# Performance work log

Hardware: AMD Instinct MI355X
Metric: run time of the kernel (lower is better)

Reference implementation:

```python
import jax, jax.numpy as jnp
import numpy as np

B, C, N, K = 8, 128, 16384, 8


def setup_inputs() -> dict:
    key = jax.random.key(0)
    ks = jax.random.split(key, 20)
    s = 1.0 / np.sqrt(C)
    def mat(k_, shape, scale):
        return jax.random.normal(k_, shape, jnp.float32) * scale
    return {
        "x": jax.random.normal(ks[0], (B, C, N, 1), jnp.float32),
        "logits": jax.random.normal(ks[1], (B, N), jnp.float32),
        "Wq1": mat(ks[2], (C, C), s), "Wk1": mat(ks[3], (C, C), s), "Wv1": mat(ks[4], (C, C), s),
        "Wq2": mat(ks[5], (C, C), s), "Wk2": mat(ks[6], (C, C), s), "Wv2": mat(ks[7], (C, C), s),
        "Wq3": mat(ks[8], (C, C), s), "Wk3": mat(ks[9], (C, C), s), "Wv3": mat(ks[10], (C, C), s),
        "ln_w": jnp.ones((C,), jnp.float32), "ln_b": jnp.zeros((C,), jnp.float32),
        "conv0_w": mat(ks[11], (C, C), s), "conv0_b": jnp.zeros((C,), jnp.float32),
        "bn_w": jnp.ones((C,), jnp.float32), "bn_b": jnp.zeros((C,), jnp.float32),
        "fc1_w": mat(ks[12], (C // 2, C), s), "fc1_b": jnp.zeros((C // 2,), jnp.float32),
        "fc2_w": mat(ks[13], (C, C // 2), 1.0 / np.sqrt(C // 2)), "fc2_b": jnp.zeros((C,), jnp.float32),
        "k": K,
    }


def _transformer(f, Wq, Wk, Wv):
    # f: [B, C, n] ; 1x1 convs over channel dim
    q = jnp.einsum('oc,bcn->bon', Wq, f)
    kk = jnp.einsum('oc,bcn->bon', Wk, f)
    v = jnp.einsum('oc,bcn->bon', Wv, f)
    temp = jnp.sqrt(jnp.asarray(f.shape[1], f.dtype))
    attn = jax.nn.softmax(jnp.einsum('bcn,bdn->bcd', q / temp, kk), axis=-1)  # [B,C,C]
    return jnp.einsum('bcd,bdn->bcn', attn, v)


def _layernorm_over_c(f, w, b):
    # f: [B, C, n]; original transposes to [B, n, C], LayerNorm(C, eps=1e-6), back
    ft = jnp.swapaxes(f, 1, 2)
    mu = ft.mean(-1, keepdims=True)
    var = ft.var(-1, keepdims=True)
    ft = (ft - mu) * jax.lax.rsqrt(var + 1e-6) * w + b
    return jnp.swapaxes(ft, 1, 2)


def reference(x, logits, Wq1, Wk1, Wv1, Wq2, Wk2, Wv2, Wq3, Wk3, Wv3,
              ln_w, ln_b, conv0_w, conv0_b, bn_w, bn_b, fc1_w, fc1_b, fc2_w, fc2_b, k):
    # --- tanh-threshold binning into k buckets ---
    w = jnp.tanh(logits)                       # [B, N]
    flag = 2.0 / k
    lows = -1.0 + flag * jnp.arange(k, dtype=x.dtype)   # [k]
    highs = lows + flag
    wb = w[None, :, :]                         # [1, B, N]
    # transforto0_1: in (l, r], and original zeros stay zero
    masks = ((wb > lows[:, None, None]) & (wb <= highs[:, None, None]) & (wb != 0)).astype(x.dtype)  # [k,B,N]
    nums = masks.sum(-1)                       # [k, B]
    nums = jnp.where(nums == 0, 1.0, nums)

    x2 = x[..., 0]                             # [B, C, N]
    # masked segment pooling (mean per bin), no channel-broadcast repeat
    pooled = jnp.einsum('bcn,kbn->bck', x2, masks)        # [B, C, k]
    feature = pooled / nums.T[:, None, :]                 # [B, C, k]

    # --- three tiny attention blocks with residual + LN ---
    for Wq, Wk, Wv in ((Wq1, Wk1, Wv1), (Wq2, Wk2, Wv2), (Wq3, Wk3, Wv3)):
        out = _transformer(feature, Wq, Wk, Wv) + feature
        feature = _layernorm_over_c(out, ln_w, ln_b)

    # --- scatter-add reconstruction: sum_i mask_i*x + mask_i*level_i ---
    total = masks.sum(0)                                  # [B, N]
    recon = x2 * total[:, None, :] + jnp.einsum('bck,kbn->bcn', feature, masks)
    result = recon[..., None]                             # [B, C, N, 1]

    # --- SE block ---
    mu_i = result.mean(axis=(2, 3), keepdims=True)
    var_i = result.var(axis=(2, 3), keepdims=True)
    h = (result - mu_i) * jax.lax.rsqrt(var_i + 1e-5)     # InstanceNorm2d
    mu_b = h.mean(axis=(0, 2, 3), keepdims=True)
    var_b = h.var(axis=(0, 2, 3), keepdims=True)
    h = (h - mu_b) * jax.lax.rsqrt(var_b + 1e-5)          # BatchNorm2d (batch stats)
    h = h * bn_w[None, :, None, None] + bn_b[None, :, None, None]
    h = jax.nn.gelu(h, approximate=False)
    conv = jnp.einsum('oc,bcnp->bonp', conv0_w, h) + conv0_b[None, :, None, None]
    sq = conv.reshape(conv.shape[0], conv.shape[1], -1).mean(-1)   # [B, C]
    f1 = jax.nn.gelu(sq @ fc1_w.T + fc1_b, approximate=False)
    f2 = jax.nn.sigmoid(f1 @ fc2_w.T + fc2_b)
    return conv * f2[:, :, None, None]
```

## Files before the change

### kernel.cpp

```cpp
#include <hip/hip_runtime.h>
#include <math.h>

#define Bdim 8
#define Cdim 128
#define Ndim 16384
#define Kdim 8

typedef __attribute__((ext_vector_type(8))) short short8;
typedef __attribute__((ext_vector_type(4))) float f32x4;

__global__ void __launch_bounds__(256) k_bin(const float* __restrict__ logits,
                                             signed char* __restrict__ kbin,
                                             int* __restrict__ cnt) {
  __shared__ int h[Kdim];
  int tid = threadIdx.x;
  if (tid < Kdim) h[tid] = 0;
  __syncthreads();
  int idx = blockIdx.x * 256 + tid;
  int b = idx >> 14;
  float w = tanhf(logits[idx]);
  int kb = -1;
#pragma unroll
  for (int j = 0; j < Kdim; ++j) {
    float lo = -1.0f + 0.25f * (float)j;
    float hi = lo + 0.25f;
    if (w > lo && w <= hi && w != 0.0f) kb = j;
  }
  kbin[idx] = (signed char)kb;
  if (kb >= 0) atomicAdd(&h[kb], 1);
  __syncthreads();
  if (tid < Kdim) atomicAdd(&cnt[b * Kdim + tid], h[tid]);
}

__global__ void __launch_bounds__(256) k_pool(const float* __restrict__ x,
                                              const signed char* __restrict__ kbin,
                                              float* __restrict__ pooled,
                                              float* __restrict__ sxx) {
  int bc = blockIdx.x;
  int b = bc >> 7;
  const float4* xr = (const float4*)(x + (size_t)bc * Ndim);
  const char4* kr = (const char4*)(kbin + b * Ndim);
  float acc[Kdim];
#pragma unroll
  for (int j = 0; j < Kdim; ++j) acc[j] = 0.f;
  float s2 = 0.f;
  int tid = threadIdx.x;
  for (int n4 = tid; n4 < Ndim / 4; n4 += 256) {
    float4 v = xr[n4];
    char4 kb = kr[n4];
    float ve[4] = {v.x, v.y, v.z, v.w};
    signed char ke[4] = {kb.x, kb.y, kb.z, kb.w};
#pragma unroll
    for (int e = 0; e < 4; ++e) {
      float xv = ve[e];
      int kv = ke[e];
      if (kv >= 0) s2 += xv * xv;
#pragma unroll
      for (int j = 0; j < Kdim; ++j) acc[j] += (kv == j) ? xv : 0.f;
    }
  }
#pragma unroll
  for (int off = 32; off > 0; off >>= 1) {
#pragma unroll
    for (int j = 0; j < Kdim; ++j) acc[j] += __shfl_down(acc[j], off);
    s2 += __shfl_down(s2, off);
  }
  __shared__ float red[4][Kdim + 1];
  int wv = tid >> 6, ln = tid & 63;
  if (ln == 0) {
#pragma unroll
    for (int j = 0; j < Kdim; ++j) red[wv][j] = acc[j];
    red[wv][Kdim] = s2;
  }
  __syncthreads();
  if (tid < Kdim) pooled[bc * Kdim + tid] = red[0][tid] + red[1][tid] + red[2][tid] + red[3][tid];
  if (tid == Kdim) sxx[bc] = red[0][Kdim] + red[1][Kdim] + red[2][Kdim] + red[3][Kdim];
}

__global__ void __launch_bounds__(256) k_warm(
    const float* __restrict__ p0, const float* __restrict__ p1, const float* __restrict__ p2,
    const float* __restrict__ p3, const float* __restrict__ p4, const float* __restrict__ p5,
    const float* __restrict__ p6, const float* __restrict__ p7, const float* __restrict__ p8,
    float* __restrict__ dummy) {
  int g = blockIdx.x >> 3;
  int t = threadIdx.x;
  int idx = g * 256 + t;
  int m = idx >> 12;
  int w = idx & 4095;
  const float* mp = m == 0 ? p0 : m == 1 ? p1 : m == 2 ? p2 : m == 3 ? p3 : m == 4 ? p4
                  : m == 5 ? p5 : m == 6 ? p6 : m == 7 ? p7 : p8;
  float4 v = ((const float4*)mp)[w];
  float s = v.x + v.y + v.z + v.w;
#pragma unroll
  for (int off = 32; off > 0; off >>= 1) s += __shfl_down(s, off);
  if ((t & 63) == 0) dummy[blockIdx.x * 4 + (t >> 6)] = s;
}

__global__ void __launch_bounds__(1024) k_xform(
    const float* __restrict__ pooled, const int* __restrict__ cnt,
    const float* __restrict__ sxx,
    const float* __restrict__ Wq1, const float* __restrict__ Wk1, const float* __restrict__ Wv1,
    const float* __restrict__ Wq2, const float* __restrict__ Wk2, const float* __restrict__ Wv2,
    const float* __restrict__ Wq3, const float* __restrict__ Wk3, const float* __restrict__ Wv3,
    const float* __restrict__ ln_w, const float* __restrict__ ln_b,
    float* __restrict__ feat, float* __restrict__ mu_i, float* __restrict__ rs_i,
    float* __restrict__ ratio) {
  __shared__ float Wl[Cdim][132];
  __shared__ float f_l[Kdim][132], q_l[Kdim][132], kk_l[Kdim][132], v_l[Kdim][132];
  __shared__ float part[Kdim][Kdim][132];
  __shared__ float pm[Kdim][132], ps[Kdim][132];
  __shared__ float lnw_l[Cdim], lnb_l[Cdim];
  __shared__ float cnt_raw[Kdim], cnt_div[Kdim];
  __shared__ float redA[Kdim][2], redB[Kdim][2];
  int b = blockIdx.x, tid = threadIdx.x;
  int c_ = tid & 127, h_ = tid >> 7;
  int o8 = tid >> 3, j8 = tid & 7;
  const float* Wq[3] = {Wq1, Wq2, Wq3};
  const float* Wk[3] = {Wk1, Wk2, Wk3};
  const float* Wv[3] = {Wv1, Wv2, Wv3};
  float4 pf0, pf1, pf2, pf3;

#define ISSUE(P)                                            \
  do {                                                      \
    const float4* s_ = (const float4*)(P);                  \
    pf0 = s_[tid]; pf1 = s_[tid + 1024];                    \
    pf2 = s_[tid + 2048]; pf3 = s_[tid + 3072];             \
  } while (0)
#define STAGE_WRITE()                                       \
  do {                                                      \
    *(float4*)&Wl[tid >> 5][(tid & 31) * 4] = pf0;          \
    *(float4*)&Wl[(tid + 1024) >> 5][(tid & 31) * 4] = pf1; \
    *(float4*)&Wl[(tid + 2048) >> 5][(tid & 31) * 4] = pf2; \
    *(float4*)&Wl[(tid + 3072) >> 5][(tid & 31) * 4] = pf3; \
  } while (0)
#define PROJ_DOT(dst)                                              \
  do {                                                             \
    float a0 = 0.f, a1 = 0.f, a2 = 0.f, a3 = 0.f;                  \
    _Pragma("unroll 4") for (int d4 = 0; d4 < 32; d4 += 4) {       \
      float4 w0 = *(const float4*)&Wl[o8][d4 * 4];                 \
      float4 f0 = *(const float4*)&f_l[j8][d4 * 4];                \
      float4 w1 = *(const float4*)&Wl[o8][d4 * 4 + 4];             \
      float4 f1 = *(const float4*)&f_l[j8][d4 * 4 + 4];            \
      float4 w2 = *(const float4*)&Wl[o8][d4 * 4 + 8];             \
      float4 f2 = *(const float4*)&f_l[j8][d4 * 4 + 8];            \
      float4 w3 = *(const float4*)&Wl[o8][d4 * 4 + 12];            \
      float4 f3 = *(const float4*)&f_l[j8][d4 * 4 + 12];           \
      a0 = fmaf(w0.x, f0.x, a0); a0 = fmaf(w0.y, f0.y, a0);        \
      a0 = fmaf(w0.z, f0.z, a0); a0 = fmaf(w0.w, f0.w, a0);        \
      a1 = fmaf(w1.x, f1.x, a1); a1 = fmaf(w1.y, f1.y, a1);        \
      a1 = fmaf(w1.z, f1.z, a1); a1 = fmaf(w1.w, f1.w, a1);        \
      a2 = fmaf(w2.x, f2.x, a2); a2 = fmaf(w2.y, f2.y, a2);        \
      a2 = fmaf(w2.z, f2.z, a2); a2 = fmaf(w2.w, f2.w, a2);        \
      a3 = fmaf(w3.x, f3.x, a3); a3 = fmaf(w3.y, f3.y, a3);        \
      a3 = fmaf(w3.z, f3.z, a3); a3 = fmaf(w3.w, f3.w, a3);        \
    }                                                              \
    dst = (a0 + a1) + (a2 + a3);                                   \
  } while (0)

  ISSUE(Wq1);
  if (tid < Kdim) {
    int cc = cnt[b * Kdim + tid];
    cnt_raw[tid] = (float)cc;
    cnt_div[tid] = (float)(cc == 0 ? 1 : cc);
  }
  if (tid >= 128 && tid < 256) lnw_l[tid - 128] = ln_w[tid - 128];
  if (tid >= 256 && tid < 384) lnb_l[tid - 256] = ln_b[tid - 256];
  __syncthreads();
  f_l[j8][o8] = pooled[(b * Cdim + o8) * Kdim + j8] / cnt_div[j8];
  const float inv_temp = 0.08838834764831845f;
  float t_carry = 0.f;
  float sv[16];
  float mloc = 0.f;
  for (int layer = 0; layer < 3; ++layer) {
    if (layer > 0) {
      float S1 = redA[h_][0] + redA[h_][1];
      float S2 = redB[h_][0] + redB[h_][1];
      float mu = S1 * (1.f / Cdim);
      float var = S2 * (1.f / Cdim) - mu * mu;
      float rs = rsqrtf(var + 1e-6f);
      f_l[h_][c_] = (t_carry - mu) * rs * lnw_l[c_] + lnb_l[c_];
    }
    STAGE_WRITE();
    ISSUE(Wk[layer]);
    __syncthreads();
    {
      float r;
      PROJ_DOT(r);
      q_l[j8][o8] = r * inv_temp;
    }
    __syncthreads();
    STAGE_WRITE();
    ISSUE(Wv[layer]);
    __syncthreads();
    {
      float r;
      PROJ_DOT(r);
      kk_l[j8][o8] = r;
    }
    __syncthreads();
    STAGE_WRITE();
    if (layer < 2) ISSUE(Wq[layer + 1]);
    __syncthreads();
    {
      float r;
      PROJ_DOT(r);
      v_l[j8][o8] = r;
    }
    __syncthreads();
    {
      int d0 = h_ * 16;
      float qv[8];
#pragma unroll
      for (int j = 0; j < 8; ++j) qv[j] = q_l[j][c_];
#pragma unroll
      for (int dd = 0; dd < 16; ++dd) sv[dd] = 0.f;
#pragma unroll
      for (int j = 0; j < 8; ++j) {
#pragma unroll
        for (int d4 = 0; d4 < 4; ++d4) {
          float4 k4 = *(const float4*)&kk_l[j][d0 + d4 * 4];
          sv[d4 * 4 + 0] = fmaf(qv[j], k4.x, sv[d4 * 4 + 0]);
          sv[d4 * 4 + 1] = fmaf(qv[j], k4.y, sv[d4 * 4 + 1]);
          sv[d4 * 4 + 2] = fmaf(qv[j], k4.z, sv[d4 * 4 + 2]);
          sv[d4 * 4 + 3] = fmaf(qv[j], k4.w, sv[d4 * 4 + 3]);
        }
      }
      mloc = sv[0];
#pragma unroll
      for (int dd = 1; dd < 16; ++dd) mloc = fmaxf(mloc, sv[dd]);
      float sl = 0.f;
#pragma unroll
      for (int dd = 0; dd < 16; ++dd) {
        sv[dd] = expf(sv[dd] - mloc);
        sl += sv[dd];
      }
      pm[h_][c_] = mloc;
      ps[h_][c_] = sl;
    }
    __syncthreads();
    {
      float M = pm[0][c_];
#pragma unroll
      for (int hh = 1; hh < 8; ++hh) M = fmaxf(M, pm[hh][c_]);
      float S = 0.f;
#pragma unroll
      for (int hh = 0; hh < 8; ++hh) S += ps[hh][c_] * expf(pm[hh][c_] - M);
      float fac = expf(mloc - M) / S;
#pragma unroll
      for (int dd = 0; dd < 16; ++dd) sv[dd] *= fac;
      int d0 = h_ * 16;
#pragma unroll
      for (int j = 0; j < 8; ++j) {
        float po = 0.f;
#pragma unroll
        for (int d4 = 0; d4 < 4; ++d4) {
          float4 v4 = *(const float4*)&v_l[j][d0 + d4 * 4];
          po = fmaf(sv[d4 * 4 + 0], v4.x, po);
          po = fmaf(sv[d4 * 4 + 1], v4.y, po);
          po = fmaf(sv[d4 * 4 + 2], v4.z, po);
          po = fmaf(sv[d4 * 4 + 3], v4.w, po);
        }
        part[h_][j][c_] = po;
      }
    }
    __syncthreads();
    {
      float t = f_l[h_][c_];
#pragma unroll
      for (int hh = 0; hh < 8; ++hh) t += part[hh][h_][c_];
      t_carry = t;
      float s1 = t, s2 = t * t;
#pragma unroll
      for (int off = 32; off > 0; off >>= 1) {
        s1 += __shfl_xor(s1, off);
        s2 += __shfl_xor(s2, off);
      }
      int wv = (tid >> 6) & 1;
      if ((tid & 63) == 0) { redA[h_][wv] = s1; redB[h_][wv] = s2; }
    }
    __syncthreads();
  }
  {
    float S1 = redA[h_][0] + redA[h_][1];
    float S2 = redB[h_][0] + redB[h_][1];
    float mu = S1 * (1.f / Cdim);
    float var = S2 * (1.f / Cdim) - mu * mu;
    float rs = rsqrtf(var + 1e-6f);
    f_l[h_][c_] = (t_carry - mu) * rs * lnw_l[c_] + lnb_l[c_];
  }
  __syncthreads();
  if (tid < Cdim) {
    int c = tid;
    float S1 = 0.f, S2c = 0.f;
#pragma unroll
    for (int j = 0; j < Kdim; ++j) {
      float pl = pooled[(b * Cdim + c) * Kdim + j];
      float fe = f_l[j][c];
      feat[(b * Cdim + c) * Kdim + j] = fe;
      S1 += pl + cnt_raw[j] * fe;
      S2c += 2.f * pl * fe + cnt_raw[j] * fe * fe;
    }
    float S2 = sxx[b * Cdim + c] + S2c;
    float mu = S1 * (1.f / Ndim);
    float var = S2 * (1.f / Ndim) - mu * mu;
    float rs = rsqrtf(var + 1e-5f);
    mu_i[b * Cdim + c] = mu;
    rs_i[b * Cdim + c] = rs;
    ratio[b * Cdim + c] = var * rs * rs;
  }
#undef ISSUE
#undef STAGE_WRITE
#undef PROJ_DOT
}

__global__ void k_alpha(const float* __restrict__ mu_i, const float* __restrict__ rs_i,
                        const float* __restrict__ ratio, const float* __restrict__ bn_w,
                        const float* __restrict__ bn_b, float* __restrict__ alpha,
                        float* __restrict__ beta) {
  int c = threadIdx.x;
  float vb = 0.f;
  for (int b = 0; b < Bdim; ++b) vb += ratio[b * Cdim + c];
  vb *= (1.f / Bdim);
  float rsb = rsqrtf(vb + 1e-5f);
  float w = bn_w[c], bb = bn_b[c];
  for (int b = 0; b < Bdim; ++b) {
    float a = rs_i[b * Cdim + c] * rsb * w;
    alpha[b * Cdim + c] = a;
    beta[b * Cdim + c] = bb - mu_i[b * Cdim + c] * a;
  }
}

__global__ void k_wsplit(const float* __restrict__ W, unsigned short* __restrict__ Wh,
                         unsigned short* __restrict__ Wl, unsigned short* __restrict__ Whs,
                         unsigned short* __restrict__ Wls) {
  int idx = blockIdx.x * 256 + threadIdx.x;
  int o = idx >> 7, c = idx & 127;
  float v = W[idx];
  unsigned u = __float_as_uint(v);
  unsigned rh = (u + 0x7FFFu + ((u >> 16) & 1u)) & 0xFFFF0000u;
  float vh = __uint_as_float(rh);
  float r = v - vh;
  unsigned u2 = __float_as_uint(r);
  unsigned rl = (u2 + 0x7FFFu + ((u2 >> 16) & 1u)) >> 16;
  unsigned short hs = (unsigned short)(rh >> 16);
  unsigned short ls = (unsigned short)rl;
  Wh[idx] = hs;
  Wl[idx] = ls;
  int pos = o * 128 + (((c >> 3) ^ (o & 7)) << 3) + (c & 7);
  Whs[pos] = hs;
  Wls[pos] = ls;
}

__global__ void __launch_bounds__(256) k_gpack(
    const float* __restrict__ x, const signed char* __restrict__ kbin,
    const float* __restrict__ feat,
    const float* __restrict__ mu_i, const float* __restrict__ rs_i,
    const float* __restrict__ ratio, const float* __restrict__ bn_w,
    const float* __restrict__ bn_b, unsigned short* __restrict__ gpack,
    float* __restrict__ gsum) {
  __shared__ unsigned short xg[Cdim][132];
  __shared__ float feat_l[Cdim][Kdim];
  __shared__ float al_l[Cdim], be_l[Cdim];
  __shared__ signed char kb_l[128];
  int tile = blockIdx.x;
  int b = tile >> 7, nb = tile & 127;
  int n0 = nb * 128;
  int t = threadIdx.x;
  for (int idx = t; idx < Cdim * Kdim; idx += 256)
    ((float*)feat_l)[idx] = feat[b * Cdim * Kdim + idx];
  if (t < 128) {
    int c = t;
    float vb = 0.f;
#pragma unroll
    for (int bb = 0; bb < Bdim; ++bb) vb += ratio[bb * Cdim + c];
    vb *= (1.f / Bdim);
    float rsb = rsqrtf(vb + 1e-5f);
    float a = rs_i[b * Cdim + c] * rsb * bn_w[c];
    al_l[c] = a;
    be_l[c] = bn_b[c] - mu_i[b * Cdim + c] * a;
    kb_l[c] = kbin[b * Ndim + n0 + c];
  }
  __syncthreads();
#pragma unroll 4
  for (int it = 0; it < 16; ++it) {
    int idx = it * 256 + t;
    int q = idx & 31, c = idx >> 5;
    float4 xv = *(const float4*)(x + ((size_t)(b * Cdim + c)) * Ndim + n0 + q * 4);
    float a = al_l[c], be = be_l[c];
    float xe[4] = {xv.x, xv.y, xv.z, xv.w};
    unsigned short rr[4];
#pragma unroll
    for (int e = 0; e < 4; ++e) {
      int kb = kb_l[q * 4 + e];
      float rec = (kb >= 0) ? (xe[e] + feat_l[c][kb]) : 0.0f;
      float h = fmaf(a, rec, be);
      float g = 0.5f * h * (1.0f + erff(h * 0.7071067811865475244f));
      unsigned u = __float_as_uint(g);
      rr[e] = (unsigned short)((u + 0x7FFFu + ((u >> 16) & 1u)) >> 16);
    }
    *(ushort4*)&xg[c][q * 4] = make_ushort4(rr[0], rr[1], rr[2], rr[3]);
  }
  __syncthreads();
  {
    int c = t >> 1, half = t & 1;
    float s = 0.f;
#pragma unroll 8
    for (int i = 0; i < 64; ++i) {
      unsigned us = xg[c][half * 64 + i];
      s += __uint_as_float(us << 16);
    }
    s += __shfl_xor(s, 1);
    if (half == 0) atomicAdd(&gsum[b * Cdim + c], s);
  }
  unsigned short* tb = gpack + (size_t)tile * 16384;
#pragma unroll 2
  for (int it = 0; it < 8; ++it) {
    int idx = it * 256 + t;
    int cg = idx & 15, n = idx >> 4;
    unsigned u32s[4];
#pragma unroll
    for (int p = 0; p < 4; ++p) {
      unsigned lo = xg[cg * 8 + 2 * p][n];
      unsigned hi = xg[cg * 8 + 2 * p + 1][n];
      u32s[p] = lo | (hi << 16);
    }
    int g = cg ^ (n & 7);
    *(uint4*)(tb + n * 128 + g * 8) = make_uint4(u32s[0], u32s[1], u32s[2], u32s[3]);
  }
}

__global__ void __launch_bounds__(256) k_gmean(
    const float* __restrict__ x, const signed char* __restrict__ kbin,
    const float* __restrict__ feat, const float* __restrict__ alpha,
    const float* __restrict__ beta, float* __restrict__ gmean) {
  int bc = blockIdx.x;
  int b = bc >> 7;
  __shared__ float fl[Kdim];
  int tid = threadIdx.x;
  if (tid < Kdim) fl[tid] = feat[bc * Kdim + tid];
  __syncthreads();
  float a = alpha[bc], be = beta[bc];
  const float4* xr = (const float4*)(x + (size_t)bc * Ndim);
  const char4* kr = (const char4*)(kbin + b * Ndim);
  float s = 0.f;
  for (int n4 = tid; n4 < Ndim / 4; n4 += 256) {
    float4 v = xr[n4];
    char4 kb = kr[n4];
    float ve[4] = {v.x, v.y, v.z, v.w};
    signed char ke[4] = {kb.x, kb.y, kb.z, kb.w};
#pragma unroll
    for (int e = 0; e < 4; ++e) {
      int kv = ke[e];
      float rec = 0.f;
#pragma unroll
      for (int j = 0; j < Kdim; ++j) rec += (kv == j) ? (ve[e] + fl[j]) : 0.f;
      float h = fmaf(a, rec, be);
      s += 0.5f * h * (1.0f + erff(h * 0.7071067811865475244f));
    }
  }
#pragma unroll
  for (int off = 32; off > 0; off >>= 1) s += __shfl_down(s, off);
  __shared__ float red[4];
  int wv = tid >> 6;
  if ((tid & 63) == 0) red[wv] = s;
  __syncthreads();
  if (tid == 0) gmean[bc] = (red[0] + red[1] + red[2] + red[3]) * (1.0f / Ndim);
}

__global__ void __launch_bounds__(128) k_mlp(const float* __restrict__ gmean,
                                             const float* __restrict__ W,
                                             const float* __restrict__ conv_b,
                                             const float* __restrict__ fc1w,
                                             const float* __restrict__ fc1b,
                                             const float* __restrict__ fc2w,
                                             const float* __restrict__ fc2b,
                                             float inv,
                                             float* __restrict__ f2g) {
  __shared__ float gm[Cdim];
  __shared__ float sq[Cdim];
  __shared__ float f1[64];
  int b = blockIdx.x, tid = threadIdx.x;
  gm[tid] = gmean[b * Cdim + tid] * inv;
  __syncthreads();
  float a = conv_b[tid];
  const float* wr = W + tid * Cdim;
  for (int c = 0; c < Cdim; ++c) a = fmaf(wr[c], gm[c], a);
  sq[tid] = a;
  __syncthreads();
  if (tid < 64) {
    float a1 = fc1b[tid];
    for (int c = 0; c < Cdim; ++c) a1 = fmaf(fc1w[tid * Cdim + c], sq[c], a1);
    f1[tid] = 0.5f * a1 * (1.0f + erff(a1 * 0.7071067811865475244f));
  }
  __syncthreads();
  float a2 = fc2b[tid];
  for (int i = 0; i < 64; ++i) a2 = fmaf(fc2w[tid * 64 + i], f1[i], a2);
  f2g[b * Cdim + tid] = 1.0f / (1.0f + expf(-a2));
}

__global__ void __launch_bounds__(1024) k_conv_g(
    const unsigned short* __restrict__ gpack,
    const unsigned short* __restrict__ Whs, const unsigned short* __restrict__ Wls,
    const float* __restrict__ bias, const float* __restrict__ f2g,
    float* __restrict__ out) {
  __shared__ unsigned short Whl[16384];
  __shared__ unsigned short Wll[16384];
  __shared__ unsigned short Bb[2][16384];
  __shared__ float bi_l[Cdim], f2_l[Cdim];
  int t = threadIdx.x;
  int blk = blockIdx.x;
  int b = blk >> 5;
  int tile0 = blk * 4;
  if (t < 128) {
    bi_l[t] = bias[t];
    f2_l[t] = f2g[b * Cdim + t];
  }
  {
    const uint4* gw = (const uint4*)Whs;
    const uint4* gl = (const uint4*)Wls;
    const uint4* gb = (const uint4*)(gpack + (size_t)tile0 * 16384);
    uint4* lw = (uint4*)Whl;
    uint4* ll = (uint4*)Wll;
    uint4* lb = (uint4*)Bb[0];
    lw[t] = gw[t]; lw[t + 1024] = gw[t + 1024];
    ll[t] = gl[t]; ll[t + 1024] = gl[t + 1024];
    lb[t] = gb[t]; lb[t + 1024] = gb[t + 1024];
  }
  __syncthreads();
  int w = t >> 6, lane = t & 63;
  int wo = (w & 1) * 64, wn = (w >> 1) * 16;
  int l15 = lane & 15, lg = lane >> 4;
  int nrow = wn + l15;
  int brow = nrow * 128;
  int bswz = nrow & 7;
  int cur = 0;
  for (int tt = 0; tt < 4; ++tt) {
    uint4 rb0, rb1;
    if (tt < 3) {
      const uint4* gb = (const uint4*)(gpack + (size_t)(tile0 + tt + 1) * 16384);
      rb0 = gb[t];
      rb1 = gb[t + 1024];
    }
    f32x4 acc[4];
#pragma unroll
    for (int of = 0; of < 4; ++of) acc[of] = (f32x4){0.f, 0.f, 0.f, 0.f};
#pragma unroll
    for (int kb = 0; kb < 4; ++kb) {
      int g = kb * 4 + lg;
      short8 bb = *(const short8*)&Bb[cur][brow + ((g ^ bswz) << 3)];
#pragma unroll
      for (int of = 0; of < 4; ++of) {
        int o = wo + of * 16 + l15;
        int apos = o * 128 + ((g ^ (o & 7)) << 3);
        short8 ah = *(const short8*)&Whl[apos];
        short8 al_ = *(const short8*)&Wll[apos];
        acc[of] = __builtin_amdgcn_mfma_f32_16x16x32_bf16(ah, bb, acc[of], 0, 0, 0);
        acc[of] = __builtin_amdgcn_mfma_f32_16x16x32_bf16(al_, bb, acc[of], 0, 0, 0);
      }
    }
    __syncthreads();
    if (tt < 3) {
      uint4* lb = (uint4*)Bb[cur ^ 1];
      lb[t] = rb0;
      lb[t + 1024] = rb1;
    }
    __syncthreads();
    int n0 = ((tile0 + tt) & 127) * 128;
#pragma unroll
    for (int of = 0; of < 4; ++of) {
#pragma unroll
      for (int r = 0; r < 4; ++r) {
        int o = wo + of * 16 + lg * 4 + r;
        out[((size_t)(b * Cdim + o)) * Ndim + n0 + wn + l15] =
            (acc[of][r] + bi_l[o]) * f2_l[o];
      }
    }
    cur ^= 1;
  }
}

__global__ void __launch_bounds__(512, 4) k_conv_x(
    const float* __restrict__ x, const signed char* __restrict__ kbin,
    const float* __restrict__ feat, const float* __restrict__ alpha,
    const float* __restrict__ beta,
    const unsigned short* __restrict__ Wh, const unsigned short* __restrict__ Wl,
    const float* __restrict__ bias, const float* __restrict__ f2g,
    float* __restrict__ out) {
  __shared__ unsigned g_hl[Cdim][132];
  __shared__ float feat_l[Cdim][Kdim];
  __shared__ float al_l[Cdim], be_l[Cdim], f2_l[Cdim], bi_l[Cdim];
  __shared__ signed char kb_l[128];
  int bx = blockIdx.x;
  int b = bx >> 7, nb = bx & 127;
  int n0 = nb * 128;
  int tid = threadIdx.x;
  for (int idx = tid; idx < Cdim * Kdim; idx += 512)
    ((float*)feat_l)[idx] = feat[b * Cdim * Kdim + idx];
  if (tid < Cdim) {
    al_l[tid] = alpha[b * Cdim + tid];
    be_l[tid] = beta[b * Cdim + tid];
    f2_l[tid] = f2g[b * Cdim + tid];
    bi_l[tid] = bias[tid];
  }
  if (tid >= 256 && tid < 384) kb_l[tid - 256] = kbin[b * Ndim + n0 + (tid - 256)];
  __syncthreads();
  for (int idx = tid; idx < Cdim * 32; idx += 512) {
    int c = idx >> 5, q4 = idx & 31;
    float4 xv = *(const float4*)(x + ((size_t)(b * Cdim + c)) * Ndim + n0 + q4 * 4);
    float a = al_l[c], be = be_l[c];
    float xe[4] = {xv.x, xv.y, xv.z, xv.w};
    unsigned r[4];
#pragma unroll
    for (int e = 0; e < 4; ++e) {
      int kb = kb_l[q4 * 4 + e];
      float rec = (kb >= 0) ? (xe[e] + feat_l[c][kb]) : 0.0f;
      float h = fmaf(a, rec, be);
      float g = 0.5f * h * (1.0f + erff(h * 0.7071067811865475244f));
      unsigned u = __float_as_uint(g);
      unsigned rh = (u + 0x7FFFu + ((u >> 16) & 1u)) & 0xFFFF0000u;
      float rr = g - __uint_as_float(rh);
      unsigned u2 = __float_as_uint(rr);
      unsigned rl = (u2 + 0x7FFFu + ((u2 >> 16) & 1u)) >> 16;
      r[e] = rh | rl;
    }
    int p4 = (q4 * 4) ^ (((c >> 3) & 1) << 4);
    *(uint4*)&g_hl[c][p4] = make_uint4(r[0], r[1], r[2], r[3]);
  }
  __syncthreads();
  int wid = tid >> 6, lane = tid & 63;
  int wo = (wid & 1) * 64;
  int wn = (wid >> 1) * 32;
  int l15 = lane & 15, lg = lane >> 4;
  f32x4 acc[4][2];
#pragma unroll
  for (int of = 0; of < 4; ++of)
#pragma unroll
    for (int nf = 0; nf < 2; ++nf) acc[of][nf] = (f32x4){0.f, 0.f, 0.f, 0.f};
#pragma unroll 2
  for (int kb = 0; kb < 4; ++kb) {
    int kbase = kb * 32 + lg * 8;
    short8 ah[4], alo[4];
#pragma unroll
    for (int of = 0; of < 4; ++of) {
      int o = wo + of * 16 + l15;
      ah[of] = *(const short8*)(Wh + o * Cdim + kbase);
      alo[of] = *(const short8*)(Wl + o * Cdim + kbase);
    }
#pragma unroll
    for (int nf = 0; nf < 2; ++nf) {
      int n = wn + nf * 16 + l15;
      int par = lg & 1;
      short8 bh, bl;
#pragma unroll
      for (int j = 0; j < 8; ++j) {
        unsigned u = g_hl[kbase + j][n ^ (par << 4)];
        bh[j] = (short)(u >> 16);
        bl[j] = (short)(u & 0xFFFFu);
      }
#pragma unroll
      for (int of = 0; of < 4; ++of) {
        acc[of][nf] = __builtin_amdgcn_mfma_f32_16x16x32_bf16(ah[of], bh, acc[of][nf], 0, 0, 0);
        acc[of][nf] = __builtin_amdgcn_mfma_f32_16x16x32_bf16(ah[of], bl, acc[of][nf], 0, 0, 0);
        acc[of][nf] = __builtin_amdgcn_mfma_f32_16x16x32_bf16(alo[of], bh, acc[of][nf], 0, 0, 0);
      }
    }
  }
#pragma unroll
  for (int of = 0; of < 4; ++of) {
#pragma unroll
    for (int nf = 0; nf < 2; ++nf) {
#pragma unroll
      for (int r = 0; r < 4; ++r) {
        int o = wo + of * 16 + lg * 4 + r;
        int n = wn + nf * 16 + l15;
        out[((size_t)(b * Cdim + o)) * Ndim + n0 + n] = (acc[of][nf][r] + bi_l[o]) * f2_l[o];
      }
    }
  }
}

extern "C" void kernel_launch(void* const* d_in, const int* in_sizes, int n_in,
                              void* d_out, int out_size, void* d_ws, size_t ws_size,
                              hipStream_t stream) {
  const float* x = (const float*)d_in[0];
  const float* logits = (const float*)d_in[1];
  const float* Wq1 = (const float*)d_in[2];
  const float* Wk1 = (const float*)d_in[3];
  const float* Wv1 = (const float*)d_in[4];
  const float* Wq2 = (const float*)d_in[5];
  const float* Wk2 = (const float*)d_in[6];
  const float* Wv2 = (const float*)d_in[7];
  const float* Wq3 = (const float*)d_in[8];
  const float* Wk3 = (const float*)d_in[9];
  const float* Wv3 = (const float*)d_in[10];
  const float* ln_w = (const float*)d_in[11];
  const float* ln_b = (const float*)d_in[12];
  const float* conv0_w = (const float*)d_in[13];
  const float* conv0_b = (const float*)d_in[14];
  const float* bn_w = (const float*)d_in[15];
  const float* bn_b = (const float*)d_in[16];
  const float* fc1_w = (const float*)d_in[17];
  const float* fc1_b = (const float*)d_in[18];
  const float* fc2_w = (const float*)d_in[19];
  const float* fc2_b = (const float*)d_in[20];
  float* out = (float*)d_out;

  char* p = (char*)d_ws;
  auto alloc = [&](size_t bytes) {
    char* r = p;
    p += (bytes + 255) & ~(size_t)255;
    return r;
  };
  signed char* kbin = (signed char*)alloc(Bdim * Ndim);
  int* cnt = (int*)alloc(Bdim * Kdim * 4);
  float* pooled = (float*)alloc(Bdim * Cdim * Kdim * 4);
  float* sxx = (float*)alloc(Bdim * Cdim * 4);
  float* feat = (float*)alloc(Bdim * Cdim * Kdim * 4);
  float* mu_i = (float*)alloc(Bdim * Cdim * 4);
  float* rs_i = (float*)alloc(Bdim * Cdim * 4);
  float* ratio = (float*)alloc(Bdim * Cdim * 4);
  float* alpha = (float*)alloc(Bdim * Cdim * 4);
  float* beta = (float*)alloc(Bdim * Cdim * 4);
  unsigned short* Wh = (unsigned short*)alloc(Cdim * Cdim * 2);
  unsigned short* Wlo = (unsigned short*)alloc(Cdim * Cdim * 2);
  unsigned short* Whs = (unsigned short*)alloc(Cdim * Cdim * 2);
  unsigned short* Wls = (unsigned short*)alloc(Cdim * Cdim * 2);
  float* f2g = (float*)alloc(Bdim * Cdim * 4);
  float* gmean = (float*)alloc(Bdim * Cdim * 4);
  float* warmdummy = (float*)alloc(1152 * 4 * 4);
  unsigned short* gpack = (unsigned short*)alloc((size_t)Bdim * Cdim * Ndim * 2);
  bool fast = ((size_t)(p - (char*)d_ws) <= ws_size);

  hipMemsetAsync(cnt, 0, Bdim * Kdim * sizeof(int), stream);
  k_bin<<<Bdim * Ndim / 256, 256, 0, stream>>>(logits, kbin, cnt);
  k_wsplit<<<Cdim * Cdim / 256, 256, 0, stream>>>(conv0_w, Wh, Wlo, Whs, Wls);
  k_pool<<<Bdim * Cdim, 256, 0, stream>>>(x, kbin, pooled, sxx);
  k_warm<<<1152, 256, 0, stream>>>(Wq1, Wk1, Wv1, Wq2, Wk2, Wv2, Wq3, Wk3, Wv3, warmdummy);
  k_xform<<<Bdim, 1024, 0, stream>>>(pooled, cnt, sxx, Wq1, Wk1, Wv1, Wq2, Wk2, Wv2,
                                     Wq3, Wk3, Wv3, ln_w, ln_b, feat, mu_i, rs_i, ratio);
  if (fast) {
    hipMemsetAsync(gmean, 0, Bdim * Cdim * sizeof(float), stream);
    k_gpack<<<Bdim * 128, 256, 0, stream>>>(x, kbin, feat, mu_i, rs_i, ratio, bn_w, bn_b,
                                            gpack, gmean);
    k_mlp<<<Bdim, 128, 0, stream>>>(gmean, conv0_w, conv0_b, fc1_w, fc1_b, fc2_w, fc2_b,
                                    1.0f / Ndim, f2g);
    k_conv_g<<<256, 1024, 0, stream>>>(gpack, Whs, Wls, conv0_b, f2g, out);
  } else {
    k_alpha<<<1, 128, 0, stream>>>(mu_i, rs_i, ratio, bn_w, bn_b, alpha, beta);
    k_gmean<<<Bdim * Cdim, 256, 0, stream>>>(x, kbin, feat, alpha, beta, gmean);
    k_mlp<<<Bdim, 128, 0, stream>>>(gmean, conv0_w, conv0_b, fc1_w, fc1_b, fc2_w, fc2_b,
                                    1.0f, f2g);
    k_conv_x<<<Bdim * (Ndim / 128), 512, 0, stream>>>(x, kbin, feat, alpha, beta, Wh, Wlo,
                                                      conv0_b, f2g, out);
  }
}
```

Baseline: 141.0 us.

## Stage all three projection weights at once as bf16 and fuse QKV dots

The per-batch transformer kernel now prefetches Wq, Wk and Wv for a layer together, rounds them to bf16 in shared memory, and computes the q, k and v projections in one fused loop. This cuts the number of block barriers per layer from six to two, and each f_l load is shared across the three dot products. Each thread now holds twelve float4 prefetch registers, which raises register pressure. Rounding the weights to bf16 adds precision loss to the projections.

```diff
diff --git a/kernel.cpp b/kernel.cpp
--- a/kernel.cpp
+++ b/kernel.cpp
@@ -8,6 +8,13 @@
 
 typedef __attribute__((ext_vector_type(8))) short short8;
 typedef __attribute__((ext_vector_type(4))) float f32x4;
+
+__device__ __forceinline__ unsigned rne16(float x) {
+  unsigned u = __float_as_uint(x);
+  return (u + 0x7FFFu + ((u >> 16) & 1u)) >> 16;
+}
+#define BF_LO(u) __uint_as_float((u) << 16)
+#define BF_HI(u) __uint_as_float((u) & 0xFFFF0000u)
 
 __global__ void __launch_bounds__(256) k_bin(const float* __restrict__ logits,
                                              signed char* __restrict__ kbin,
@@ -105,10 +112,10 @@
     const float* __restrict__ ln_w, const float* __restrict__ ln_b,
     float* __restrict__ feat, float* __restrict__ mu_i, float* __restrict__ rs_i,
     float* __restrict__ ratio) {
-  __shared__ float Wl[Cdim][132];
+  __shared__ unsigned short Wb[3][Cdim][132];
   __shared__ float f_l[Kdim][132], q_l[Kdim][132], kk_l[Kdim][132], v_l[Kdim][132];
-  __shared__ float part[Kdim][Kdim][132];
-  __shared__ float pm[Kdim][132], ps[Kdim][132];
+  __shared__ float part[Kdim][Kdim][Cdim];
+  __shared__ float pm[Kdim][Cdim], ps[Kdim][Cdim];
   __shared__ float lnw_l[Cdim], lnb_l[Cdim];
   __shared__ float cnt_raw[Kdim], cnt_div[Kdim];
   __shared__ float redA[Kdim][2], redB[Kdim][2];
@@ -118,46 +125,36 @@
   const float* Wq[3] = {Wq1, Wq2, Wq3};
   const float* Wk[3] = {Wk1, Wk2, Wk3};
   const float* Wv[3] = {Wv1, Wv2, Wv3};
-  float4 pf0, pf1, pf2, pf3;
-
-#define ISSUE(P)                                            \
+  float4 pf[12];
+
+#define ISSUE3(L)                                           \
   do {                                                      \
-    const float4* s_ = (const float4*)(P);                  \
-    pf0 = s_[tid]; pf1 = s_[tid + 1024];                    \
-    pf2 = s_[tid + 2048]; pf3 = s_[tid + 3072];             \
+    const float4* sq_ = (const float4*)Wq[L];               \
+    const float4* sk_ = (const float4*)Wk[L];               \
+    const float4* sv_ = (const float4*)Wv[L];               \
+    pf[0] = sq_[tid]; pf[1] = sq_[tid + 1024];              \
+    pf[2] = sq_[tid + 2048]; pf[3] = sq_[tid + 3072];       \
+    pf[4] = sk_[tid]; pf[5] = sk_[tid + 1024];              \
+    pf[6] = sk_[tid + 2048]; pf[7] = sk_[tid + 3072];       \
+    pf[8] = sv_[tid]; pf[9] = sv_[tid + 1024];              \
+    pf[10] = sv_[tid + 2048]; pf[11] = sv_[tid + 3072];     \
   } while (0)
-#define STAGE_WRITE()                                       \
-  do {                                                      \
-    *(float4*)&Wl[tid >> 5][(tid & 31) * 4] = pf0;          \
-    *(float4*)&Wl[(tid + 1024) >> 5][(tid & 31) * 4] = pf1; \
-    *(float4*)&Wl[(tid + 2048) >> 5][(tid & 31) * 4] = pf2; \
-    *(float4*)&Wl[(tid + 3072) >> 5][(tid & 31) * 4] = pf3; \
+#define STAGE3()                                                       \
+  do {                                                                 \
+    _Pragma("unroll") for (int m = 0; m < 3; ++m) {                    \
+      _Pragma("unroll") for (int k = 0; k < 4; ++k) {                  \
+        int idx = tid + k * 1024;                                      \
+        int r = idx >> 5, q = idx & 31;                                \
+        float4 v = pf[m * 4 + k];                                      \
+        unsigned a0 = rne16(v.x), a1 = rne16(v.y);                     \
+        unsigned a2 = rne16(v.z), a3 = rne16(v.w);                     \
+        *(uint2*)&Wb[m][r][q * 4] =                                    \
+            make_uint2(a0 | (a1 << 16), a2 | (a3 << 16));              \
+      }                                                                \
+    }                                                                  \
   } while (0)
-#define PROJ_DOT(dst)                                              \
-  do {                                                             \
-    float a0 = 0.f, a1 = 0.f, a2 = 0.f, a3 = 0.f;                  \
-    _Pragma("unroll 4") for (int d4 = 0; d4 < 32; d4 += 4) {       \
-      float4 w0 = *(const float4*)&Wl[o8][d4 * 4];                 \
-      float4 f0 = *(const float4*)&f_l[j8][d4 * 4];                \
-      float4 w1 = *(const float4*)&Wl[o8][d4 * 4 + 4];             \
-      float4 f1 = *(const float4*)&f_l[j8][d4 * 4 + 4];            \
-      float4 w2 = *(const float4*)&Wl[o8][d4 * 4 + 8];             \
-      float4 f2 = *(const float4*)&f_l[j8][d4 * 4 + 8];            \
-      float4 w3 = *(const float4*)&Wl[o8][d4 * 4 + 12];            \
-      float4 f3 = *(const float4*)&f_l[j8][d4 * 4 + 12];           \
-      a0 = fmaf(w0.x, f0.x, a0); a0 = fmaf(w0.y, f0.y, a0);        \
-      a0 = fmaf(w0.z, f0.z, a0); a0 = fmaf(w0.w, f0.w, a0);        \
-      a1 = fmaf(w1.x, f1.x, a1); a1 = fmaf(w1.y, f1.y, a1);        \
-      a1 = fmaf(w1.z, f1.z, a1); a1 = fmaf(w1.w, f1.w, a1);        \
-      a2 = fmaf(w2.x, f2.x, a2); a2 = fmaf(w2.y, f2.y, a2);        \
-      a2 = fmaf(w2.z, f2.z, a2); a2 = fmaf(w2.w, f2.w, a2);        \
-      a3 = fmaf(w3.x, f3.x, a3); a3 = fmaf(w3.y, f3.y, a3);        \
-      a3 = fmaf(w3.z, f3.z, a3); a3 = fmaf(w3.w, f3.w, a3);        \
-    }                                                              \
-    dst = (a0 + a1) + (a2 + a3);                                   \
-  } while (0)
-
-  ISSUE(Wq1);
+
+  ISSUE3(0);
   if (tid < Kdim) {
     int cc = cnt[b * Kdim + tid];
     cnt_raw[tid] = (float)cc;
@@ -180,31 +177,37 @@
       float rs = rsqrtf(var + 1e-6f);
       f_l[h_][c_] = (t_carry - mu) * rs * lnw_l[c_] + lnb_l[c_];
     }
-    STAGE_WRITE();
-    ISSUE(Wk[layer]);
+    STAGE3();
+    if (layer < 2) ISSUE3(layer + 1);
     __syncthreads();
     {
-      float r;
-      PROJ_DOT(r);
-      q_l[j8][o8] = r * inv_temp;
-    }
-    __syncthreads();
-    STAGE_WRITE();
-    ISSUE(Wv[layer]);
-    __syncthreads();
-    {
-      float r;
-      PROJ_DOT(r);
-      kk_l[j8][o8] = r;
-    }
-    __syncthreads();
-    STAGE_WRITE();
-    if (layer < 2) ISSUE(Wq[layer + 1]);
-    __syncthreads();
-    {
-      float r;
-      PROJ_DOT(r);
-      v_l[j8][o8] = r;
+      float aq0 = 0.f, aq1 = 0.f, ak0 = 0.f, ak1 = 0.f, av0 = 0.f, av1 = 0.f;
+#pragma unroll
+      for (int d8 = 0; d8 < 16; ++d8) {
+        uint2 q0 = *(const uint2*)&Wb[0][o8][d8 * 8];
+        uint2 q1 = *(const uint2*)&Wb[0][o8][d8 * 8 + 4];
+        uint2 k0 = *(const uint2*)&Wb[1][o8][d8 * 8];
+        uint2 k1 = *(const uint2*)&Wb[1][o8][d8 * 8 + 4];
+        uint2 v0 = *(const uint2*)&Wb[2][o8][d8 * 8];
+        uint2 v1 = *(const uint2*)&Wb[2][o8][d8 * 8 + 4];
+        float4 fa = *(const float4*)&f_l[j8][d8 * 8];
+        float4 fb = *(const float4*)&f_l[j8][d8 * 8 + 4];
+        aq0 = fmaf(BF_LO(q0.x), fa.x, aq0); aq1 = fmaf(BF_HI(q0.x), fa.y, aq1);
+        aq0 = fmaf(BF_LO(q0.y), fa.z, aq0); aq1 = fmaf(BF_HI(q0.y), fa.w, aq1);
+        aq0 = fmaf(BF_LO(q1.x), fb.x, aq0); aq1 = fmaf(BF_HI(q1.x), fb.y, aq1);
+        aq0 = fmaf(BF_LO(q1.y), fb.z, aq0); aq1 = fmaf(BF_HI(q1.y), fb.w, aq1);
+        ak0 = fmaf(BF_LO(k0.x), fa.x, ak0); ak1 = fmaf(BF_HI(k0.x), fa.y, ak1);
+        ak0 = fmaf(BF_LO(k0.y), fa.z, ak0); ak1 = fmaf(BF_HI(k0.y), fa.w, ak1);
+        ak0 = fmaf(BF_LO(k1.x), fb.x, ak0); ak1 = fmaf(BF_HI(k1.x), fb.y, ak1);
+        ak0 = fmaf(BF_LO(k1.y), fb.z, ak0); ak1 = fmaf(BF_HI(k1.y), fb.w, ak1);
+        av0 = fmaf(BF_LO(v0.x), fa.x, av0); av1 = fmaf(BF_HI(v0.x), fa.y, av1);
+        av0 = fmaf(BF_LO(v0.y), fa.z, av0); av1 = fmaf(BF_HI(v0.y), fa.w, av1);
+        av0 = fmaf(BF_LO(v1.x), fb.x, av0); av1 = fmaf(BF_HI(v1.x), fb.y, av1);
+        av0 = fmaf(BF_LO(v1.y), fb.z, av0); av1 = fmaf(BF_HI(v1.y), fb.w, av1);
+      }
+      q_l[j8][o8] = (aq0 + aq1) * inv_temp;
+      kk_l[j8][o8] = ak0 + ak1;
+      v_l[j8][o8] = av0 + av1;
     }
     __syncthreads();
     {
@@ -308,9 +311,8 @@
     rs_i[b * Cdim + c] = rs;
     ratio[b * Cdim + c] = var * rs * rs;
   }
-#undef ISSUE
-#undef STAGE_WRITE
-#undef PROJ_DOT
+#undef ISSUE3
+#undef STAGE3
 }
 
 __global__ void k_alpha(const float* __restrict__ mu_i, const float* __restrict__ rs_i,
```

Result: slower. 169.5 us (+20.2%).
